# Kernel optimization log

Hardware: AMD Instinct MI355X
Metric: run time of the kernel (lower is better)

## Reference

```python
import jax, jax.numpy as jnp
import numpy as np

B, S, D, H = 2, 4096, 512, 8
HD = D // H  # head_dim = 64


def setup_inputs() -> dict:
    key = jax.random.key(0)
    ks = jax.random.split(key, 7)
    scale = 1.0 / np.sqrt(D)
    return {
        "x": jax.random.normal(ks[0], (B, S, D), dtype=jnp.float32),
        "Wq": jax.random.uniform(ks[1], (D, D), jnp.float32, -scale, scale),
        "bq": jax.random.uniform(ks[2], (D,), jnp.float32, -scale, scale),
        "Wk": jax.random.uniform(ks[3], (D, D), jnp.float32, -scale, scale),
        "bk": jax.random.uniform(ks[4], (D,), jnp.float32, -scale, scale),
        "Wv": jax.random.uniform(ks[5], (D, D), jnp.float32, -scale, scale),
        "bv": jax.random.uniform(ks[6], (D,), jnp.float32, -scale, scale),
    }


def reference(x, Wq, bq, Wk, bk, Wv, bv):
    # torch Linear: y = x @ W.T + b
    q = x @ Wq.T + bq  # [B,S,D]
    k = x @ Wk.T + bk
    v = x @ Wv.T + bv
    # split heads -> [B,H,S,HD]
    q = q.reshape(B, S, H, HD).transpose(0, 2, 1, 3)
    k = k.reshape(B, S, H, HD).transpose(0, 2, 1, 3)
    v = v.reshape(B, S, H, HD).transpose(0, 2, 1, 3)
    # NOTE: module scales by sqrt(pitch_dim), NOT sqrt(head_dim) -- keep faithful.
    scores = jnp.einsum("bhqd,bhkd->bhqk", q, k) / jnp.sqrt(jnp.float32(D))
    causal = jnp.tril(jnp.ones((S, S), dtype=bool))  # lower-tri incl. diag allowed
    scores = jnp.where(causal, scores, -jnp.inf)
    attn = jax.nn.softmax(scores, axis=-1)
    out = jnp.einsum("bhqk,bhkd->bhqd", attn, v)  # [B,H,S,HD]
    return out.transpose(0, 2, 1, 3).reshape(B, S, D)
```

## Files before the change

kernel.cpp:

```cpp
#include <hip/hip_runtime.h>
#include <hip/hip_bf16.h>
#include <math.h>

#define BB 2
#define SS 4096
#define DD 512
#define HH 8
#define HD 64
#define MSD (BB*SS*DD)
#define WSZ (DD*DD)

#define WOFF (5*(size_t)MSD)
#define POFF (3*(size_t)MSD)

typedef __attribute__((ext_vector_type(8))) short bf16x8;
typedef __attribute__((ext_vector_type(4))) float f32x4;

__device__ __forceinline__ unsigned short f2bf(float f) {
    unsigned int u = __float_as_uint(f);
    u += 0x7fff + ((u >> 16) & 1);
    return (unsigned short)(u >> 16);
}
__device__ __forceinline__ unsigned int pk2bf(float a, float b) {
    __hip_bfloat162 h = __float22bfloat162_rn(make_float2(a, b));
    union { __hip_bfloat162 h2; unsigned int u; } cv; cv.h2 = h;
    return cv.u;
}
__device__ __forceinline__ bf16x8 cvt8(const float4& a, const float4& b) {
    unsigned int wv[4] = { pk2bf(a.x, a.y), pk2bf(a.z, a.w),
                           pk2bf(b.x, b.y), pk2bf(b.z, b.w) };
    return *(const bf16x8*)wv;
}

#define GLD16(gsrc, ldst) \
    __builtin_amdgcn_global_load_lds((const __attribute__((address_space(1))) unsigned int*)(gsrc), \
                                     (__attribute__((address_space(3))) unsigned int*)(ldst), 16, 0, 0)

#define CH(qb,t0,t1) ((unsigned)(qb) | ((unsigned)(t0)<<8) | ((unsigned)(t1)<<16))
__device__ __constant__ unsigned int SCHED[48] = {
  CH(31,0,32),  CH(31,32,64), CH(0,0,2),
  CH(15,0,32),  CH(29,0,30),  CH(1,0,4),
  CH(29,30,60), CH(14,0,30),  CH(2,0,6),
  CH(28,0,29),  CH(28,29,58), CH(3,0,8),
  CH(27,0,28),  CH(13,0,28),  CH(4,0,10),
  CH(26,0,27),  CH(26,27,54), CH(5,0,12),
  CH(25,0,26),  CH(12,0,26),  CH(6,0,14),
  CH(24,0,25),  CH(24,25,50), CH(7,0,16),
  CH(30,0,31),  CH(17,0,18),  CH(16,0,17),
  CH(30,31,62), CH(17,18,36), CH(16,17,34),
  CH(27,28,56), CH(19,0,20),  CH(8,0,18),
  CH(25,26,52), CH(20,0,21),  CH(18,0,19),
  CH(23,0,24),  CH(22,0,23),  CH(18,19,38),
  CH(23,24,48), CH(21,0,22),  CH(19,20,40),
  CH(11,0,24),  CH(21,22,44), CH(9,0,20),
  CH(22,23,46), CH(10,0,22),  CH(20,21,42),
};

__global__ __launch_bounds__(256)
void convert_w(const float* __restrict__ Wq, const float* __restrict__ Wk,
               const float* __restrict__ Wv, unsigned short* __restrict__ ws) {
    const int i8 = blockIdx.x*256 + threadIdx.x;
    size_t o = (size_t)i8 * 8;
    const int wsel = (int)(o / WSZ);
    const float* src = (wsel == 0) ? Wq : (wsel == 1) ? Wk : Wv;
    unsigned short* dst = ws + WOFF + (size_t)wsel*WSZ;
    const size_t off = o % WSZ;
    float4 a = *(const float4*)&src[off];
    float4 b = *(const float4*)&src[off+4];
    *(bf16x8*)&dst[off] = cvt8(a, b);
}

__global__ __launch_bounds__(512, 2)
void qkv_fused(const float* __restrict__ x,
               const float* __restrict__ bq, const float* __restrict__ bk,
               const float* __restrict__ bv, unsigned short* __restrict__ ws) {
    const unsigned short* Wz0 = ws + WOFF;
    const unsigned short* Wz1 = ws + WOFF + WSZ;
    const unsigned short* Wz2 = ws + WOFF + 2*(size_t)WSZ;

    __shared__ __align__(16) unsigned short As[2][128*64];
    __shared__ __align__(16) unsigned short Bs[3][2][128*64];

    const int tid  = threadIdx.x;
    const int w    = tid >> 6, l = tid & 63;
    const int quad = l >> 4,  r16 = l & 15;
    const int wm   = w >> 2,  wn  = w & 3;
    const int n0   = blockIdx.x * 128;
    const int m0   = blockIdx.y * 128;

    const int sr8 = l >> 3, sc = l & 7;

    f32x4 acc[3][4][2];
    #pragma unroll
    for (int z = 0; z < 3; ++z)
        #pragma unroll
        for (int i = 0; i < 4; ++i)
            #pragma unroll
            for (int j = 0; j < 2; ++j) acc[z][i][j] = (f32x4){0.f,0.f,0.f,0.f};

    const int arow0 = w*16 +     sr8;
    const int arow1 = w*16 + 8 + sr8;
    const float* xa0 = x + (size_t)(m0 + arow0)*DD + (sc ^ (arow0 & 7))*8;
    const float* xa1 = x + (size_t)(m0 + arow1)*DD + (sc ^ (arow1 & 7))*8;
    unsigned short* da0[2] = { &As[0][arow0*64 + sc*8], &As[1][arow0*64 + sc*8] };
    unsigned short* da1[2] = { &As[0][arow1*64 + sc*8], &As[1][arow1*64 + sc*8] };

    auto STAGE_B = [&](int k0, int b) {
        #pragma unroll
        for (int u = 0; u < 2; ++u) {
            const int r0  = w*16 + u*8;
            const int row = r0 + sr8;
            const int c   = sc ^ (row & 7);
            GLD16(&Wz0[(size_t)(n0 + row)*DD + k0 + c*8], &Bs[0][b][r0*64]);
            GLD16(&Wz1[(size_t)(n0 + row)*DD + k0 + c*8], &Bs[1][b][r0*64]);
            GLD16(&Wz2[(size_t)(n0 + row)*DD + k0 + c*8], &Bs[2][b][r0*64]);
        }
    };

    STAGE_B(0, 0);
    float4 ra[4];
    ra[0] = *(const float4*)xa0; ra[1] = *(const float4*)(xa0+4);
    ra[2] = *(const float4*)xa1; ra[3] = *(const float4*)(xa1+4);
    xa0 += 64; xa1 += 64;

    #pragma unroll
    for (int kt = 0; kt < 8; ++kt) {
        __syncthreads();

        const int bb = kt & 1;
        *(bf16x8*)da0[bb] = cvt8(ra[0], ra[1]);
        *(bf16x8*)da1[bb] = cvt8(ra[2], ra[3]);

        __syncthreads();

        if (kt + 1 < 8) {
            STAGE_B((kt + 1)*64, (kt + 1) & 1);
            ra[0] = *(const float4*)xa0; ra[1] = *(const float4*)(xa0+4);
            ra[2] = *(const float4*)xa1; ra[3] = *(const float4*)(xa1+4);
            xa0 += 64; xa1 += 64;
        }

        #pragma unroll
        for (int kc = 0; kc < 2; ++kc) {
            bf16x8 a[4];
            #pragma unroll
            for (int i = 0; i < 4; ++i) {
                const int mr = wm*64 + i*16 + r16;
                a[i] = *(const bf16x8*)&As[bb][mr*64 + (((kc*4+quad) ^ (mr&7))*8)];
            }
            bf16x8 b0[2], b1[2], b2[2];
            #pragma unroll
            for (int j = 0; j < 2; ++j) {
                const int nr = wn*32 + j*16 + r16;
                const int sw = ((kc*4+quad) ^ (nr&7))*8;
                b0[j] = *(const bf16x8*)&Bs[0][bb][nr*64 + sw];
                b1[j] = *(const bf16x8*)&Bs[1][bb][nr*64 + sw];
                b2[j] = *(const bf16x8*)&Bs[2][bb][nr*64 + sw];
            }
            __builtin_amdgcn_s_setprio(1);
            #pragma unroll
            for (int i = 0; i < 4; ++i)
                #pragma unroll
                for (int j = 0; j < 2; ++j) {
                    acc[0][i][j] = __builtin_amdgcn_mfma_f32_16x16x32_bf16(b0[j], a[i], acc[0][i][j], 0, 0, 0);
                    acc[1][i][j] = __builtin_amdgcn_mfma_f32_16x16x32_bf16(b1[j], a[i], acc[1][i][j], 0, 0, 0);
                    acc[2][i][j] = __builtin_amdgcn_mfma_f32_16x16x32_bf16(a[i], b2[j], acc[2][i][j], 0, 0, 0);
                }
            __builtin_amdgcn_s_setprio(0);
        }
    }

    __syncthreads();
    unsigned short* Ct = &As[0][0];
    const float qscale = 0.04419417382415922f * 1.4426950408889634f;
    const float* biases[3] = { bq, bk, bv };

    #pragma unroll
    for (int z = 0; z < 3; ++z) {
        unsigned short* dst = ws + (size_t)z*MSD;
        const float* bias = biases[z];

        if (z == 2) {
            #pragma unroll
            for (int j = 0; j < 2; ++j) {
                const int nloc = wn*32 + j*16 + r16;
                const float bz = bias[n0 + nloc];
                #pragma unroll
                for (int i = 0; i < 4; ++i) {
                    const int chunk = wm*8 + i*2 + (quad>>1);
                    const int off   = (quad & 1) * 4;
                    unsigned short r4[4];
                    #pragma unroll
                    for (int reg = 0; reg < 4; ++reg)
                        r4[reg] = f2bf(acc[2][i][j][reg] + bz);
                    *(uint2*)&Ct[nloc*128 + ((chunk ^ (nloc & 7))*8) + off] = *(const uint2*)r4;
                }
            }
        } else {
            #pragma unroll
            for (int j = 0; j < 2; ++j) {
                const int nbase = wn*32 + j*16 + quad*4;
                const float4 bz4 = *(const float4*)&bias[n0 + nbase];
                const int chunk = wn*4 + j*2 + (quad>>1);
                const int off   = (quad & 1) * 4;
                #pragma unroll
                for (int i = 0; i < 4; ++i) {
                    const int mloc = wm*64 + i*16 + r16;
                    float v0 = acc[z][i][j][0] + bz4.x;
                    float v1 = acc[z][i][j][1] + bz4.y;
                    float v2 = acc[z][i][j][2] + bz4.z;
                    float v3 = acc[z][i][j][3] + bz4.w;
                    if (z == 0) { v0 *= qscale; v1 *= qscale; v2 *= qscale; v3 *= qscale; }
                    unsigned short r4[4] = { f2bf(v0), f2bf(v1), f2bf(v2), f2bf(v3) };
                    *(uint2*)&Ct[mloc*128 + ((chunk ^ (mloc & 7))*8) + off] = *(const uint2*)r4;
                }
            }
        }
        __syncthreads();

        if (z == 2) {
            const int b_ = m0 >> 12, s0_ = m0 & (SS-1);
            #pragma unroll
            for (int p = 0; p < 4; ++p) {
                const int f = p*512 + tid;
                const int nrow = f >> 4;
                const int mch  = f & 15;
                bf16x8 v = *(const bf16x8*)&Ct[nrow*128 + ((mch ^ (nrow & 7))*8)];
                const int ng = n0 + nrow;
                const int h = ng >> 6, hd = ng & 63;
                *(bf16x8*)&dst[((size_t)(b_*HH + h)*HD + hd)*SS + s0_ + mch*8] = v;
            }
        } else {
            #pragma unroll
            for (int p = 0; p < 4; ++p) {
                const int f = p*512 + tid;
                const int hh  = f >> 10;
                const int rem = f & 1023;
                const int sr  = rem >> 3;
                const int ch  = rem & 7;
                bf16x8 v = *(const bf16x8*)&Ct[sr*128 + (((hh*8 + ch) ^ (sr & 7))*8)];
                const int mg = m0 + sr;
                const int b_ = mg >> 12, s_ = mg & (SS-1);
                const int hg = (n0 >> 6) + hh;
                *(bf16x8*)&dst[((size_t)(b_*HH + hg)*SS + s_)*HD + ch*8] = v;
            }
        }
        if (z < 2) __syncthreads();
    }
}

__global__ __launch_bounds__(256, 4)
void attn_mfma(unsigned short* __restrict__ ws, float* __restrict__ out) {
    const int bx = blockIdx.x;
    const int k_ = bx >> 8;
    const int j_ = bx & 255;
    const int bh = j_ & 15;
    const int ti = j_ >> 4;
    const unsigned int e = SCHED[ti*3 + k_];
    const int qb = e & 255;
    const int t0 = (e >> 8) & 255;
    const int t1 = (e >> 16) & 255;
    const int split = !(t0 == 0 && t1 == 2*qb + 2);
    const int half  = (t0 != 0);

    const int tid  = threadIdx.x;
    const int w    = tid >> 6, l = tid & 63;
    const int quad = l >> 4,  r16 = l & 15;
    const int qlo  = qb*128 + w*32;
    const int tdiag = 2*qb + (w >> 1);
    const int qoff  = 32*(w & 1);

    const unsigned short* Qg  = ws;
    const unsigned short* Kg  = ws + (size_t)MSD;
    const unsigned short* Vtg = ws + 2*(size_t)MSD;

    __shared__ __align__(16) unsigned short Ks[2][64*64];
    __shared__ __align__(16) unsigned short Vs[2][64*64];

    const size_t kbase = (size_t)bh*SS*HD;
    const size_t vbase = (size_t)bh*HD*SS;

    bf16x8 bqf[2][2];
    #pragma unroll
    for (int nt = 0; nt < 2; ++nt)
        #pragma unroll
        for (int kc = 0; kc < 2; ++kc)
            bqf[nt][kc] = *(const bf16x8*)&Qg[kbase + (size_t)(qlo + nt*16 + r16)*HD + kc*32 + quad*8];

    const f32x4 ZZ = (f32x4){0.f,0.f,0.f,0.f};
    const unsigned short onep[8] = {0x3F80,0x3F80,0x3F80,0x3F80,0x3F80,0x3F80,0x3F80,0x3F80};
    const bf16x8 ones8 = *(const bf16x8*)onep;

    f32x4 od[4][2];
    #pragma unroll
    for (int mt = 0; mt < 4; ++mt)
        #pragma unroll
        for (int nt = 0; nt < 2; ++nt) od[mt][nt] = ZZ;
    f32x4 lacc[2] = {ZZ, ZZ};

    const int x7 = r16 & 7;
    const unsigned short* pK0 = &Ks[0][r16*64 + ((quad     ^ x7)*8)];
    const unsigned short* pK1 = &Ks[0][r16*64 + (((4+quad) ^ x7)*8)];
    const unsigned short* pV0 = &Vs[0][r16*64 + ((quad     ^ x7)*8)];
    const unsigned short* pV1 = &Vs[0][r16*64 + (((4+quad) ^ x7)*8)];

    const int sr8 = l >> 3, sc = l & 7;
    const int row0 = w*16 + sr8,     row1 = w*16 + 8 + sr8;
    const int c0   = sc ^ (row0 & 7), c1  = sc ^ (row1 & 7);
    const unsigned short* kg0 = Kg  + kbase + (size_t)(t0*64 + row0)*HD + c0*8;
    const unsigned short* kg1 = Kg  + kbase + (size_t)(t0*64 + row1)*HD + c1*8;
    const unsigned short* vg0 = Vtg + vbase + (size_t)row0*SS + t0*64 + c0*8;
    const unsigned short* vg1 = Vtg + vbase + (size_t)row1*SS + t0*64 + c1*8;
    unsigned short* lk0 = &Ks[0][(w*16    )*64];
    unsigned short* lk1 = &Ks[0][(w*16 + 8)*64];
    unsigned short* lv0 = &Vs[0][(w*16    )*64];
    unsigned short* lv1 = &Vs[0][(w*16 + 8)*64];

    GLD16(kg0, lk0); GLD16(kg1, lk1);
    GLD16(vg0, lv0); GLD16(vg1, lv1);
    kg0 += 64*HD; kg1 += 64*HD; vg0 += 64; vg1 += 64;

    for (int t = t0; t < t1; ++t) {
        __syncthreads();

        if (t + 1 < t1) {
            const int d1 = ((t + 1 - t0) & 1) * 4096;
            GLD16(kg0, lk0 + d1); GLD16(kg1, lk1 + d1);
            GLD16(vg0, lv0 + d1); GLD16(vg1, lv1 + d1);
            kg0 += 64*HD; kg1 += 64*HD; vg0 += 64; vg1 += 64;
        }

        if (t <= tdiag) {
            const int boff = ((t - t0) & 1) * 4096;

            f32x4 z[4][2];
            __builtin_amdgcn_s_setprio(1);
            #pragma unroll
            for (int mt = 0; mt < 4; ++mt) {
                bf16x8 ak0 = *(const bf16x8*)(pK0 + boff + mt*1024);
                bf16x8 ak1 = *(const bf16x8*)(pK1 + boff + mt*1024);
                #pragma unroll
                for (int nt = 0; nt < 2; ++nt) {
                    z[mt][nt] = __builtin_amdgcn_mfma_f32_16x16x32_bf16(ak0, bqf[nt][0], ZZ, 0, 0, 0);
                    z[mt][nt] = __builtin_amdgcn_mfma_f32_16x16x32_bf16(ak1, bqf[nt][1], z[mt][nt], 0, 0, 0);
                }
            }
            __builtin_amdgcn_s_setprio(0);

            if (t == tdiag) {
                #pragma unroll
                for (int mt = 0; mt < 4; ++mt)
                    #pragma unroll
                    for (int nt = 0; nt < 2; ++nt)
                        #pragma unroll
                        for (int reg = 0; reg < 4; ++reg)
                            if (mt*16 + quad*4 + reg > qoff + nt*16 + r16)
                                z[mt][nt][reg] = -1e30f;
            }

            unsigned int X0[4][2], X1[4][2];
            #pragma unroll
            for (int mt = 0; mt < 4; ++mt)
                #pragma unroll
                for (int nt = 0; nt < 2; ++nt) {
                    X0[mt][nt] = pk2bf(__builtin_amdgcn_exp2f(z[mt][nt][0]),
                                       __builtin_amdgcn_exp2f(z[mt][nt][1]));
                    X1[mt][nt] = pk2bf(__builtin_amdgcn_exp2f(z[mt][nt][2]),
                                       __builtin_amdgcn_exp2f(z[mt][nt][3]));
                }

            bf16x8 pf[2][2];
            #pragma unroll
            for (int nt = 0; nt < 2; ++nt)
                #pragma unroll
                for (int kc = 0; kc < 2; ++kc) {
                    unsigned int a0 = X0[2*kc][nt], b0 = X0[2*kc+1][nt];
                    unsigned int a1 = X1[2*kc][nt], b1 = X1[2*kc+1][nt];
                    asm("v_permlane32_swap_b32 %0, %1" : "+v"(a0), "+v"(b0));
                    asm("v_permlane16_swap_b32 %0, %1" : "+v"(a0), "+v"(b0));
                    asm("v_permlane32_swap_b32 %0, %1" : "+v"(a1), "+v"(b1));
                    asm("v_permlane16_swap_b32 %0, %1" : "+v"(a1), "+v"(b1));
                    unsigned int wv[4] = { a0, a1, b0, b1 };
                    pf[nt][kc] = *(const bf16x8*)wv;
                }

            __builtin_amdgcn_s_setprio(1);
            #pragma unroll
            for (int nt = 0; nt < 2; ++nt) {
                lacc[nt] = __builtin_amdgcn_mfma_f32_16x16x32_bf16(ones8, pf[nt][0], lacc[nt], 0, 0, 0);
                lacc[nt] = __builtin_amdgcn_mfma_f32_16x16x32_bf16(ones8, pf[nt][1], lacc[nt], 0, 0, 0);
            }
            #pragma unroll
            for (int mt = 0; mt < 4; ++mt) {
                bf16x8 av0 = *(const bf16x8*)(pV0 + boff + mt*1024);
                bf16x8 av1 = *(const bf16x8*)(pV1 + boff + mt*1024);
                #pragma unroll
                for (int nt = 0; nt < 2; ++nt) {
                    od[mt][nt] = __builtin_amdgcn_mfma_f32_16x16x32_bf16(av0, pf[nt][0], od[mt][nt], 0, 0, 0);
                    od[mt][nt] = __builtin_amdgcn_mfma_f32_16x16x32_bf16(av1, pf[nt][1], od[mt][nt], 0, 0, 0);
                }
            }
            __builtin_amdgcn_s_setprio(0);
        }
    }

    if (split) {
        const int p = 2*(bh*16 + (qb - 16)) + half;
        float* Op = (float*)(ws + POFF) + (size_t)p*(128*64);
        float* Lp = (float*)(ws + WOFF) + p*128;
        #pragma unroll
        for (int nt = 0; nt < 2; ++nt) {
            const int qloc = w*32 + nt*16 + r16;
            if (quad == 0) Lp[qloc] = lacc[nt][0];
            #pragma unroll
            for (int mt = 0; mt < 4; ++mt)
                *(f32x4*)&Op[(size_t)qloc*64 + mt*16 + quad*4] = od[mt][nt];
        }
    } else {
        const int b_ = bh >> 3, h = bh & 7;
        #pragma unroll
        for (int nt = 0; nt < 2; ++nt) {
            const float inv = 1.0f / lacc[nt][0];
            const int q = qlo + nt*16 + r16;
            float* op = out + ((size_t)(b_*SS + q))*DD + h*HD;
            #pragma unroll
            for (int mt = 0; mt < 4; ++mt) {
                float4 tt;
                tt.x = od[mt][nt][0]*inv; tt.y = od[mt][nt][1]*inv;
                tt.z = od[mt][nt][2]*inv; tt.w = od[mt][nt][3]*inv;
                *(float4*)&op[mt*16 + quad*4] = tt;
            }
        }
    }
}

__global__ __launch_bounds__(256)
void attn_combine(const unsigned short* __restrict__ ws, float* __restrict__ out) {
    const int i  = blockIdx.x*256 + threadIdx.x;
    const int d4 = i & 15;
    const int q  = (i >> 4) & 127;
    const int r  = i >> 11;
    const int bh = r >> 4, qb = 16 + (r & 15);

    const float* Opart = (const float*)(ws + POFF);
    const float* Lpart = (const float*)(ws + WOFF);

    const float4 a = *(const float4*)&Opart[((size_t)(2*r)*128 + q)*64 + d4*4];
    const float4 b = *(const float4*)&Opart[((size_t)(2*r + 1)*128 + q)*64 + d4*4];
    const float lt = Lpart[(2*r)*128 + q] + Lpart[(2*r + 1)*128 + q];
    const float inv = 1.0f / lt;

    const int qg = qb*128 + q;
    const int b_ = bh >> 3, h = bh & 7;
    float4 o;
    o.x = (a.x + b.x)*inv; o.y = (a.y + b.y)*inv;
    o.z = (a.z + b.z)*inv; o.w = (a.w + b.w)*inv;
    *(float4*)&out[((size_t)(b_*SS + qg))*DD + h*HD + d4*4] = o;
}

extern "C" void kernel_launch(void* const* d_in, const int* in_sizes, int n_in,
                              void* d_out, int out_size, void* d_ws, size_t ws_size,
                              hipStream_t stream) {
    const float* x  = (const float*)d_in[0];
    const float* Wq = (const float*)d_in[1];
    const float* bq = (const float*)d_in[2];
    const float* Wk = (const float*)d_in[3];
    const float* bk = (const float*)d_in[4];
    const float* Wv = (const float*)d_in[5];
    const float* bv = (const float*)d_in[6];
    float* out = (float*)d_out;
    unsigned short* ws = (unsigned short*)d_ws;

    convert_w<<<384, 256, 0, stream>>>(Wq, Wk, Wv, ws);

    dim3 ggrid(DD/128, (BB*SS)/128);
    qkv_fused<<<ggrid, 512, 0, stream>>>(x, bq, bk, bv, ws);

    attn_mfma<<<768, 256, 0, stream>>>(ws, out);
    attn_combine<<<2048, 256, 0, stream>>>(ws, out);
}
```

Before: 151.9 us.

## Fuse split-KV combine into attention kernel via atomic last-arriver counter

Removes the separate attn_combine launch. Each split attention block writes its partial O and row-sum, then bumps an atomic counter. The counter is stored in the first output word of its tile and zeroed by convert_w. The second block to arrive reads its partner's partial and writes the normalized final output. This saves one kernel launch and a global read/write pass, at the cost of an atomic, thread fences and a dependence on memory ordering between blocks.

```diff
diff --git a/kernel.cpp b/kernel.cpp
--- a/kernel.cpp
+++ b/kernel.cpp
@@ -58,7 +58,8 @@
 
 __global__ __launch_bounds__(256)
 void convert_w(const float* __restrict__ Wq, const float* __restrict__ Wk,
-               const float* __restrict__ Wv, unsigned short* __restrict__ ws) {
+               const float* __restrict__ Wv, unsigned short* __restrict__ ws,
+               float* __restrict__ out) {
     const int i8 = blockIdx.x*256 + threadIdx.x;
     size_t o = (size_t)i8 * 8;
     const int wsel = (int)(o / WSZ);
@@ -68,6 +69,13 @@
     float4 a = *(const float4*)&src[off];
     float4 b = *(const float4*)&src[off+4];
     *(bf16x8*)&dst[off] = cvt8(a, b);
+
+    if (blockIdx.x == 0) {
+        const int t  = threadIdx.x;
+        const int bh = t >> 4, qb = 16 + (t & 15);
+        const int b_ = bh >> 3, h = bh & 7;
+        ((unsigned int*)out)[((size_t)(b_*SS + qb*128))*DD + h*HD] = 0u;
+    }
 }
 
 __global__ __launch_bounds__(512, 2)
@@ -276,6 +284,7 @@
 
     __shared__ __align__(16) unsigned short Ks[2][64*64];
     __shared__ __align__(16) unsigned short Vs[2][64*64];
+    __shared__ unsigned int oldsh;
 
     const size_t kbase = (size_t)bh*SS*HD;
     const size_t vbase = (size_t)bh*HD*SS;
@@ -404,20 +413,51 @@
         }
     }
 
+    const int b_ = bh >> 3, h = bh & 7;
     if (split) {
-        const int p = 2*(bh*16 + (qb - 16)) + half;
-        float* Op = (float*)(ws + POFF) + (size_t)p*(128*64);
-        float* Lp = (float*)(ws + WOFF) + p*128;
+        const int r    = bh*16 + (qb - 16);
+        const int slot = 2*r + half;
+        float* Op  = (float*)(ws + POFF) + (size_t)slot*(128*64);
+        float* Lsf = (float*)(ws + WOFF) + slot*128;
+        unsigned int* cntp = (unsigned int*)(out + ((size_t)(b_*SS + qb*128))*DD + h*HD);
+
         #pragma unroll
         for (int nt = 0; nt < 2; ++nt) {
             const int qloc = w*32 + nt*16 + r16;
-            if (quad == 0) Lp[qloc] = lacc[nt][0];
+            if (quad == 0) Lsf[qloc] = lacc[nt][0];
             #pragma unroll
             for (int mt = 0; mt < 4; ++mt)
                 *(f32x4*)&Op[(size_t)qloc*64 + mt*16 + quad*4] = od[mt][nt];
         }
+        __syncthreads();
+        if (tid == 0) {
+            __threadfence();
+            oldsh = atomicAdd(cntp, 1u);
+        }
+        __syncthreads();
+        if (oldsh == 1) {
+            __threadfence();
+            const int pslot = 2*r + (1 - half);
+            const float* Pp = (const float*)(ws + POFF) + (size_t)pslot*(128*64);
+            const float* Lp = (const float*)(ws + WOFF) + pslot*128;
+            #pragma unroll
+            for (int nt = 0; nt < 2; ++nt) {
+                const int qloc = w*32 + nt*16 + r16;
+                const float inv = 1.0f / (lacc[nt][0] + Lp[qloc]);
+                float* op = out + ((size_t)(b_*SS + qb*128 + qloc))*DD + h*HD;
+                #pragma unroll
+                for (int mt = 0; mt < 4; ++mt) {
+                    f32x4 pv = *(const f32x4*)&Pp[(size_t)qloc*64 + mt*16 + quad*4];
+                    float4 tt;
+                    tt.x = (od[mt][nt][0] + pv[0])*inv;
+                    tt.y = (od[mt][nt][1] + pv[1])*inv;
+                    tt.z = (od[mt][nt][2] + pv[2])*inv;
+                    tt.w = (od[mt][nt][3] + pv[3])*inv;
+                    *(float4*)&op[mt*16 + quad*4] = tt;
+                }
+            }
+        }
     } else {
-        const int b_ = bh >> 3, h = bh & 7;
         #pragma unroll
         for (int nt = 0; nt < 2; ++nt) {
             const float inv = 1.0f / lacc[nt][0];
@@ -432,30 +472,6 @@
             }
         }
     }
-}
-
-__global__ __launch_bounds__(256)
-void attn_combine(const unsigned short* __restrict__ ws, float* __restrict__ out) {
-    const int i  = blockIdx.x*256 + threadIdx.x;
-    const int d4 = i & 15;
-    const int q  = (i >> 4) & 127;
-    const int r  = i >> 11;
-    const int bh = r >> 4, qb = 16 + (r & 15);
-
-    const float* Opart = (const float*)(ws + POFF);
-    const float* Lpart = (const float*)(ws + WOFF);
-
-    const float4 a = *(const float4*)&Opart[((size_t)(2*r)*128 + q)*64 + d4*4];
-    const float4 b = *(const float4*)&Opart[((size_t)(2*r + 1)*128 + q)*64 + d4*4];
-    const float lt = Lpart[(2*r)*128 + q] + Lpart[(2*r + 1)*128 + q];
-    const float inv = 1.0f / lt;
-
-    const int qg = qb*128 + q;
-    const int b_ = bh >> 3, h = bh & 7;
-    float4 o;
-    o.x = (a.x + b.x)*inv; o.y = (a.y + b.y)*inv;
-    o.z = (a.z + b.z)*inv; o.w = (a.w + b.w)*inv;
-    *(float4*)&out[((size_t)(b_*SS + qg))*DD + h*HD + d4*4] = o;
 }
 
 extern "C" void kernel_launch(void* const* d_in, const int* in_sizes, int n_in,
@@ -471,11 +487,10 @@
     float* out = (float*)d_out;
     unsigned short* ws = (unsigned short*)d_ws;
 
-    convert_w<<<384, 256, 0, stream>>>(Wq, Wk, Wv, ws);
+    convert_w<<<384, 256, 0, stream>>>(Wq, Wk, Wv, ws, out);
 
     dim3 ggrid(DD/128, (BB*SS)/128);
     qkv_fused<<<ggrid, 512, 0, stream>>>(x, bq, bk, bv, ws);
 
     attn_mfma<<<768, 256, 0, stream>>>(ws, out);
-    attn_combine<<<2048, 256, 0, stream>>>(ws, out);
-}
+}
```

After: 198.0 us. 30.3% more time.
